# Kernel optimization log

Measured on AMD Instinct MI355X. Metric: run time of the kernel, lower is better.

The kernel has to match this reference:

```python
import jax, jax.numpy as jnp
import numpy as np

EMBED_DIM = 768
NUM_HEADS = 12
LN_EPS = 1e-5


def _apply_rope3d(p16, e):
    """3-axis RoPE. p16: [B,1,L,3] float16 coords; e: [B,H,L,D] float32.
    Heads split into 3 groups (x/y/z); within each group last dim split in halves
    and rotated by angle coord*freqs (computed in fp16, matching the .half() cast)."""
    B, H, L, D = e.shape
    half = D // 2
    freqs = (10000.0 ** (-jnp.arange(half, dtype=jnp.float32) / half)).astype(jnp.float16)
    ang = p16[..., None] * freqs                     # [B,1,L,3,half] fp16
    ang = jnp.transpose(ang, (0, 3, 1, 2, 4))        # [B,3,1,L,half]
    c, s = jnp.cos(ang), jnp.sin(ang)                # fp16
    eg = e.reshape(B, 3, H // 3, L, D)               # 3 head groups
    e1, e2 = eg[..., :half], eg[..., half:]
    o1 = e1 * c - e2 * s                             # fp16*fp32 -> fp32
    o2 = e2 * c + e1 * s
    return jnp.concatenate([o1, o2], axis=-1).reshape(B, H, L, D)


def setup_inputs() -> dict:
    key = jax.random.key(0)
    ks = jax.random.split(key, 5)
    B, L, C = 4, 2048, EMBED_DIM
    feat = jax.random.normal(ks[0], (B, L, C), dtype=jnp.float32)
    pos = jax.random.normal(ks[1], (B, L, 3), dtype=jnp.float32)
    w_qkv = jax.random.normal(ks[2], (C, 3 * C), dtype=jnp.float32) * (1.0 / np.sqrt(C))
    b_qkv = jnp.zeros((3 * C,), dtype=jnp.float32)
    w_proj = jax.random.normal(ks[3], (C, C), dtype=jnp.float32) * (1.0 / np.sqrt(C))
    b_proj = jnp.zeros((C,), dtype=jnp.float32)
    ln_g = jnp.ones((C,), dtype=jnp.float32)
    ln_b = jnp.zeros((C,), dtype=jnp.float32)
    return {"feat": feat, "pos": pos, "ln_g": ln_g, "ln_b": ln_b,
            "w_qkv": w_qkv, "b_qkv": b_qkv, "w_proj": w_proj, "b_proj": b_proj}


def reference(feat, pos, ln_g, ln_b, w_qkv, b_qkv, w_proj, b_proj):
    B, L, C = feat.shape
    H = NUM_HEADS
    D = C // H
    # LayerNorm
    mu = jnp.mean(feat, axis=-1, keepdims=True)
    var = jnp.mean(jnp.square(feat - mu), axis=-1, keepdims=True)
    x = (feat - mu) * jax.lax.rsqrt(var + LN_EPS) * ln_g + ln_b
    # QKV projection and head split
    qkv = x @ w_qkv + b_qkv
    q, k, v = jnp.split(qkv, 3, axis=-1)
    q = q.reshape(B, L, H, D).transpose(0, 2, 1, 3)  # [B,H,L,D]
    k = k.reshape(B, L, H, D).transpose(0, 2, 1, 3)
    v = v.reshape(B, L, H, D).transpose(0, 2, 1, 3)
    # 3D-coordinate RoPE (angles in fp16 per original .half() cast)
    p16 = pos.astype(jnp.float16)[:, None]           # [B,1,L,3]
    q = _apply_rope3d(p16, q)
    k = _apply_rope3d(p16, k)
    # flex_attention with block_mask=None -> full softmax attention, scale 1/sqrt(D)
    scale = 1.0 / np.sqrt(D)
    att = jax.nn.softmax(jnp.einsum('bhqd,bhkd->bhqk', q, k) * scale, axis=-1)
    out = jnp.einsum('bhqk,bhkd->bhqd', att, v)
    out = out.transpose(0, 2, 1, 3).reshape(B, L, C)
    # output projection (dropout = identity in eval)
    return out @ w_proj + b_proj
```

## Files before the change

### kernel.cpp

```cpp
#include <hip/hip_runtime.h>

typedef unsigned short u16;
typedef unsigned int u32;
typedef __attribute__((ext_vector_type(8))) __bf16 bf16x8;
typedef __attribute__((ext_vector_type(4))) __bf16 bf16x4;
typedef __attribute__((ext_vector_type(8))) u16 ushort8;
typedef __attribute__((ext_vector_type(4))) float f32x4;

#define DEV static __device__ __forceinline__

DEV float bf2f(u16 v) { union { u32 u; float f; } x; x.u = ((u32)v) << 16; return x.f; }
DEV u16 f2bf(float f) {
  u32 u = __builtin_bit_cast(u32, f);
  return (u16)((u + 0x7fffu + ((u >> 16) & 1u)) >> 16);
}
DEV float rnd_bf(float f) { return bf2f(f2bf(f)); }
DEV u32 pack2(float a, float b) { return (u32)f2bf(a) | ((u32)f2bf(b) << 16); }

DEV void gload_lds16(const void* g, void* l) {
  __builtin_amdgcn_global_load_lds((const __attribute__((address_space(1))) u32*)g,
                                   (__attribute__((address_space(3))) u32*)l, 16, 0, 0);
}

DEV f32x4 MFMA16(bf16x8 a, bf16x8 b, f32x4 c) {
  return __builtin_amdgcn_mfma_f32_16x16x32_bf16(a, b, c, 0, 0, 0);
}

__global__ __launch_bounds__(256) void wt_transpose(const float* __restrict__ W, u16* __restrict__ Wt,
                                                    int rows, int cols) {
  __shared__ u16 t[64][65];
  const int tid = threadIdx.x;
  const int tr = blockIdx.y << 6, tc = blockIdx.x << 6;
  {
    int r = tid >> 2, c0 = (tid & 3) << 4;
    const float* src = W + (size_t)(tr + r) * cols + tc + c0;
#pragma unroll
    for (int i = 0; i < 16; i += 4) {
      float4 v = *(const float4*)(src + i);
      t[r][c0 + i]     = f2bf(v.x);
      t[r][c0 + i + 1] = f2bf(v.y);
      t[r][c0 + i + 2] = f2bf(v.z);
      t[r][c0 + i + 3] = f2bf(v.w);
    }
  }
  __syncthreads();
  {
    int dd = tid >> 2, l0 = (tid & 3) << 4;
    ushort8 o0, o1;
#pragma unroll
    for (int i = 0; i < 8; ++i) { o0[i] = t[l0 + i][dd]; o1[i] = t[l0 + 8 + i][dd]; }
    u16* dst = Wt + (size_t)(tc + dd) * rows + tr + l0;
    *(ushort8*)dst = o0;
    *(ushort8*)(dst + 8) = o1;
  }
}

__global__ __launch_bounds__(256) void ln_kernel(const float* __restrict__ feat, const float* __restrict__ gam,
                                                 const float* __restrict__ bet, u16* __restrict__ xo) {
  const int row = blockIdx.x * 4 + (threadIdx.x >> 6);
  const int lane = threadIdx.x & 63;
  const float* f = feat + (size_t)row * 768 + lane * 4;
  float4 v0 = *(const float4*)f;
  float4 v1 = *(const float4*)(f + 256);
  float4 v2 = *(const float4*)(f + 512);
  float s = v0.x + v0.y + v0.z + v0.w + v1.x + v1.y + v1.z + v1.w + v2.x + v2.y + v2.z + v2.w;
  float s2 = v0.x*v0.x + v0.y*v0.y + v0.z*v0.z + v0.w*v0.w
           + v1.x*v1.x + v1.y*v1.y + v1.z*v1.z + v1.w*v1.w
           + v2.x*v2.x + v2.y*v2.y + v2.z*v2.z + v2.w*v2.w;
#pragma unroll
  for (int off = 32; off > 0; off >>= 1) { s += __shfl_xor(s, off); s2 += __shfl_xor(s2, off); }
  const float mu = s * (1.0f / 768.0f);
  const float rstd = rsqrtf(s2 * (1.0f / 768.0f) - mu * mu + 1e-5f);
  u16* o = xo + (size_t)row * 768 + lane * 4;
  const float4* gp = (const float4*)(gam + lane * 4);
  const float4* bp = (const float4*)(bet + lane * 4);
  float4 vv[3] = {v0, v1, v2};
#pragma unroll
  for (int jj = 0; jj < 3; ++jj) {
    float4 gg = gp[jj * 64];
    float4 bb = bp[jj * 64];
    uint2 pk;
    pk.x = pack2((vv[jj].x - mu) * rstd * gg.x + bb.x, (vv[jj].y - mu) * rstd * gg.y + bb.y);
    pk.y = pack2((vv[jj].z - mu) * rstd * gg.z + bb.z, (vv[jj].w - mu) * rstd * gg.w + bb.w);
    *(uint2*)(o + jj * 256) = pk;
  }
}

template<bool F32OUT>
__global__ __launch_bounds__(256) void gemm_bt(const u16* __restrict__ A, const u16* __restrict__ Bt,
                                               const float* __restrict__ bias, void* __restrict__ Cout,
                                               int M, int N, int K) {
  __shared__ u16 lds[16384];
  const int tid = threadIdx.x;
  const int lane = tid & 63, wv = tid >> 6;
  const int l16 = lane & 15, g = lane >> 4;
  const int nt = N >> 7;
  const int bm = blockIdx.x / nt, bn = blockIdx.x % nt;
  const int m0 = bm << 7, n0 = bn << 7;
  const int wr = (wv >> 1) << 6, wc = (wv & 1) << 6;
  const int rl = wv * 8 + (lane >> 3);
  const int slot = lane & 7;

  f32x4 acc[4][4] = {};

  for (int k0 = 0; k0 < K; k0 += 64) {
    __syncthreads();
#pragma unroll
    for (int it = 0; it < 4; ++it) {
      int r = it * 32 + rl;
      gload_lds16(A + (size_t)(m0 + r) * K + k0 + 8 * (slot ^ (r & 7)),
                  (char*)lds + it * 4096 + wv * 1024);
      gload_lds16(Bt + (size_t)(n0 + r) * K + k0 + 8 * (slot ^ (r & 7)),
                  (char*)lds + 16384 + it * 4096 + wv * 1024);
    }
    __syncthreads();
#pragma unroll
    for (int ks = 0; ks < 2; ++ks) {
      bf16x8 af[4], bfr[4];
#pragma unroll
      for (int mf = 0; mf < 4; ++mf) {
        int r = wr + mf * 16 + l16;
        af[mf] = *(const bf16x8*)((const char*)lds + r * 128 + ((ks * 64 + g * 16) ^ ((r & 7) << 4)));
      }
#pragma unroll
      for (int nf = 0; nf < 4; ++nf) {
        int r = wc + nf * 16 + l16;
        bfr[nf] = *(const bf16x8*)((const char*)lds + 16384 + r * 128 + ((ks * 64 + g * 16) ^ ((r & 7) << 4)));
      }
#pragma unroll
      for (int mf = 0; mf < 4; ++mf)
#pragma unroll
        for (int nf = 0; nf < 4; ++nf)
          acc[mf][nf] = MFMA16(af[mf], bfr[nf], acc[mf][nf]);
    }
  }
#pragma unroll
  for (int nf = 0; nf < 4; ++nf) {
    int col = n0 + wc + nf * 16 + l16;
    float bb = bias[col];
#pragma unroll
    for (int mf = 0; mf < 4; ++mf) {
      int row = m0 + wr + mf * 16 + g * 4;
#pragma unroll
      for (int j = 0; j < 4; ++j) {
        float v = acc[mf][nf][j] + bb;
        if (F32OUT) ((float*)Cout)[(size_t)(row + j) * N + col] = rnd_bf(v);
        else        ((u16*)Cout)[(size_t)(row + j) * N + col] = f2bf(v);
      }
    }
  }
}

__global__ __launch_bounds__(256) void rope_qk(const u16* __restrict__ qkv, const float* __restrict__ pos,
                                               u16* __restrict__ Q, u16* __restrict__ K) {
  int gid = blockIdx.x * 256 + threadIdx.x;
  int d = gid & 31;
  int hh = (gid >> 5) % 12;
  int bl = (gid >> 5) / 12;
  const u16* row = qkv + (size_t)bl * 2304;
  float q1 = bf2f(row[hh * 64 + d]);
  float q2 = bf2f(row[hh * 64 + 32 + d]);
  float k1 = bf2f(row[768 + hh * 64 + d]);
  float k2 = bf2f(row[768 + hh * 64 + 32 + d]);
  float p = pos[(size_t)bl * 3 + (hh >> 2)];
  float fr = exp2f((float)d * -0.41524101186092029f);
  _Float16 ah = (_Float16)p * (_Float16)fr;
  float af = (float)ah;
  float sn, cs;
  sincosf(af, &sn, &cs);
  float c = (float)(_Float16)cs;
  float s = (float)(_Float16)sn;
  size_t oidx = ((size_t)((bl >> 11) * 12 + hh) * 2048 + (bl & 2047)) * 64 + d;
  Q[oidx]      = f2bf((q1 * c - q2 * s) * 0.125f);
  Q[oidx + 32] = f2bf((q2 * c + q1 * s) * 0.125f);
  K[oidx]      = f2bf(k1 * c - k2 * s);
  K[oidx + 32] = f2bf(k2 * c + k1 * s);
}

__global__ __launch_bounds__(256) void v_transpose(const u16* __restrict__ qkv, u16* __restrict__ Vt) {
  __shared__ u16 t[64][65];
  const int tid = threadIdx.x;
  const int lt = blockIdx.x, bh = blockIdx.y;
  const int b = bh / 12, h = bh - b * 12;
  {
    int r = tid >> 2, c0 = (tid & 3) << 4;
    const u16* src = qkv + (size_t)(b * 2048 + lt * 64 + r) * 2304 + 1536 + h * 64 + c0;
    ushort8 a0 = *(const ushort8*)src;
    ushort8 a1 = *(const ushort8*)(src + 8);
#pragma unroll
    for (int i = 0; i < 8; ++i) { t[r][c0 + i] = a0[i]; t[r][c0 + 8 + i] = a1[i]; }
  }
  __syncthreads();
  {
    int dd = tid >> 2, l0 = (tid & 3) << 4;
    ushort8 o0, o1;
#pragma unroll
    for (int i = 0; i < 8; ++i) { o0[i] = t[l0 + i][dd]; o1[i] = t[l0 + 8 + i][dd]; }
    u16* dst = Vt + (size_t)(bh * 64 + dd) * 2048 + lt * 64 + l0;
    *(ushort8*)dst = o0;
    *(ushort8*)(dst + 8) = o1;
  }
}

__global__ __launch_bounds__(256) void attn_kernel(const u16* __restrict__ Q, const u16* __restrict__ K,
                                                   const u16* __restrict__ Vt, u16* __restrict__ O) {
  __shared__ u16 kv_lds[2][8192];
  const int tid = threadIdx.x;
  const int lane = tid & 63, wv = tid >> 6;
  const int l16 = lane & 15, g = lane >> 4;
  const int bh = blockIdx.y;
  const int q0 = blockIdx.x * 128 + wv * 32;
  const size_t base = (size_t)bh * (2048 * 64);
  const size_t vbase = (size_t)bh * (64 * 2048);
  const int rl = wv * 8 + (lane >> 3);
  const int slot = lane & 7;

  bf16x8 qf[2][2];
#pragma unroll
  for (int qm = 0; qm < 2; ++qm)
#pragma unroll
    for (int ks = 0; ks < 2; ++ks)
      qf[qm][ks] = *(const bf16x8*)(Q + base + (size_t)(q0 + qm * 16 + l16) * 64 + ks * 32 + g * 8);

  float lsum[2] = {0.f, 0.f};
  f32x4 oacc[2][4] = {};

#pragma unroll
  for (int it = 0; it < 2; ++it) {
    int r = it * 32 + rl;
    gload_lds16(K + base + (size_t)r * 64 + 8 * (slot ^ (r & 7)),
                (char*)kv_lds + it * 4096 + wv * 1024);
    gload_lds16(Vt + vbase + (size_t)r * 2048 + 8 * (slot ^ (r & 7)),
                (char*)kv_lds + 8192 + it * 4096 + wv * 1024);
  }
  __syncthreads();

  int cur = 0;
  for (int kv0 = 0; kv0 < 2048; kv0 += 64) {
    if (kv0 + 64 < 2048) {
#pragma unroll
      for (int it = 0; it < 2; ++it) {
        int r = it * 32 + rl;
        gload_lds16(K + base + (size_t)(kv0 + 64 + r) * 64 + 8 * (slot ^ (r & 7)),
                    (char*)kv_lds + (cur ^ 1) * 16384 + it * 4096 + wv * 1024);
        gload_lds16(Vt + vbase + (size_t)r * 2048 + kv0 + 64 + 8 * (slot ^ (r & 7)),
                    (char*)kv_lds + (cur ^ 1) * 16384 + 8192 + it * 4096 + wv * 1024);
      }
    }

    const char* kb = (const char*)kv_lds + cur * 16384;
    const char* vbuf = kb + 8192;

    f32x4 st[2][4] = {};
#pragma unroll
    for (int ks = 0; ks < 2; ++ks) {
      bf16x8 kf[4];
#pragma unroll
      for (int n = 0; n < 4; ++n) {
        int r = n * 16 + l16;
        kf[n] = *(const bf16x8*)(kb + r * 128 + ((ks * 64 + g * 16) ^ ((r & 7) << 4)));
      }
      __builtin_amdgcn_s_setprio(1);
#pragma unroll
      for (int qm = 0; qm < 2; ++qm)
#pragma unroll
        for (int n = 0; n < 4; ++n)
          st[qm][n] = MFMA16(kf[n], qf[qm][ks], st[qm][n]);
      __builtin_amdgcn_s_setprio(0);
    }

#pragma unroll
    for (int ks2 = 0; ks2 < 2; ++ks2) {
      bf16x8 vf[4];
#pragma unroll
      for (int db = 0; db < 4; ++db) {
        int r = db * 16 + l16;
        int swz = (r & 7) << 4;
        const char* rowb = vbuf + r * 128;
        bf16x4 lo = *(const bf16x4*)(rowb + ((ks2 * 64 + g * 8) ^ swz));
        bf16x4 hi = *(const bf16x4*)(rowb + ((ks2 * 64 + g * 8 + 32) ^ swz));
        vf[db] = __builtin_shufflevector(lo, hi, 0, 1, 2, 3, 4, 5, 6, 7);
      }
      bf16x8 pf[2];
#pragma unroll
      for (int qm = 0; qm < 2; ++qm) {
        float e[8];
#pragma unroll
        for (int j = 0; j < 4; ++j) {
          e[j]     = __expf(st[qm][2 * ks2][j]);
          e[4 + j] = __expf(st[qm][2 * ks2 + 1][j]);
        }
        lsum[qm] += ((e[0] + e[1]) + (e[2] + e[3])) + ((e[4] + e[5]) + (e[6] + e[7]));
        ushort8 pp;
#pragma unroll
        for (int j = 0; j < 8; ++j) pp[j] = f2bf(e[j]);
        pf[qm] = __builtin_bit_cast(bf16x8, pp);
      }
      __builtin_amdgcn_s_setprio(1);
#pragma unroll
      for (int qm = 0; qm < 2; ++qm)
#pragma unroll
        for (int db = 0; db < 4; ++db)
          oacc[qm][db] = MFMA16(vf[db], pf[qm], oacc[qm][db]);
      __builtin_amdgcn_s_setprio(0);
    }

    __syncthreads();
    cur ^= 1;
  }

  const int b = bh / 12, h = bh - b * 12;
#pragma unroll
  for (int qm = 0; qm < 2; ++qm) {
    float tot = lsum[qm];
    tot += __shfl_xor(tot, 16);
    tot += __shfl_xor(tot, 32);
    float inv = 1.0f / tot;
    size_t row = (size_t)b * 2048 + q0 + qm * 16 + l16;
#pragma unroll
    for (int db = 0; db < 4; ++db) {
      uint2 pk;
      pk.x = pack2(oacc[qm][db][0] * inv, oacc[qm][db][1] * inv);
      pk.y = pack2(oacc[qm][db][2] * inv, oacc[qm][db][3] * inv);
      *(uint2*)(O + row * 768 + h * 64 + db * 16 + g * 4) = pk;
    }
  }
}

extern "C" void kernel_launch(void* const* d_in, const int* in_sizes, int n_in,
                              void* d_out, int out_size, void* d_ws, size_t ws_size,
                              hipStream_t stream) {
  (void)in_sizes; (void)n_in; (void)out_size; (void)ws_size;
  const float* feat   = (const float*)d_in[0];
  const float* pos    = (const float*)d_in[1];
  const float* ln_g   = (const float*)d_in[2];
  const float* ln_b   = (const float*)d_in[3];
  const float* w_qkv  = (const float*)d_in[4];
  const float* b_qkv  = (const float*)d_in[5];
  const float* w_proj = (const float*)d_in[6];
  const float* b_proj = (const float*)d_in[7];
  float* out = (float*)d_out;
  char* ws = (char*)d_ws;
  u16* xln    = (u16*)(ws);
  u16* wqkvT  = (u16*)(ws + 12582912);
  u16* wprojT = (u16*)(ws + 16121856);
  u16* qkv    = (u16*)(ws + 17301504);
  u16* Kb     = (u16*)(ws + 55050240);
  u16* Vtb    = (u16*)(ws + 67633152);
  u16* Qb     = xln;
  u16* attnout = qkv;

  wt_transpose<<<dim3(36, 12), 256, 0, stream>>>(w_qkv, wqkvT, 768, 2304);
  wt_transpose<<<dim3(12, 12), 256, 0, stream>>>(w_proj, wprojT, 768, 768);
  ln_kernel<<<2048, 256, 0, stream>>>(feat, ln_g, ln_b, xln);
  gemm_bt<false><<<1152, 256, 0, stream>>>(xln, wqkvT, b_qkv, qkv, 8192, 2304, 768);
  rope_qk<<<12288, 256, 0, stream>>>(qkv, pos, Qb, Kb);
  v_transpose<<<dim3(32, 48), 256, 0, stream>>>(qkv, Vtb);
  attn_kernel<<<dim3(16, 48), 256, 0, stream>>>(Qb, Kb, Vtb, attnout);
  gemm_bt<true><<<384, 256, 0, stream>>>(attnout, wprojT, b_proj, out, 8192, 768, 768);
}
```

Measured before the change: 180.3 us.

## Fuse RoPE into QKV GEMM epilogue, triple-buffer attention K/V loads, use exp2

Removes the separate rope_qk kernel by applying bias, 3D RoPE and the Q scale, with log2e folded in, inside the QKV GEMM epilogue. The attention kernel now reads Q and K directly from the strided qkv buffer. K/V staging goes from double to triple buffering with explicit vmcnt waits and raw barriers, so loads for tile t+2 are in flight while tile t is computed. exp becomes exp2 and the bf16 conversion uses the native cast. The costs are more LDS per block, strided K loads with a 2304-element row pitch, and sincos work repeated across the epilogue lanes.

```diff
diff --git a/kernel.cpp b/kernel.cpp
--- a/kernel.cpp
+++ b/kernel.cpp
@@ -25,6 +25,8 @@
 DEV f32x4 MFMA16(bf16x8 a, bf16x8 b, f32x4 c) {
   return __builtin_amdgcn_mfma_f32_16x16x32_bf16(a, b, c, 0, 0, 0);
 }
+
+#define QSCALE (0.125f * 1.442695040888963f)
 
 __global__ __launch_bounds__(256) void wt_transpose(const float* __restrict__ W, u16* __restrict__ Wt,
                                                     int rows, int cols) {
@@ -86,10 +88,10 @@
   }
 }
 
-template<bool F32OUT>
+template<bool ROPE, bool F32OUT>
 __global__ __launch_bounds__(256) void gemm_bt(const u16* __restrict__ A, const u16* __restrict__ Bt,
                                                const float* __restrict__ bias, void* __restrict__ Cout,
-                                               int M, int N, int K) {
+                                               const float* __restrict__ pos, int M, int N, int K) {
   __shared__ u16 lds[16384];
   const int tid = threadIdx.x;
   const int lane = tid & 63, wv = tid >> 6;
@@ -134,47 +136,59 @@
           acc[mf][nf] = MFMA16(af[mf], bfr[nf], acc[mf][nf]);
     }
   }
-#pragma unroll
-  for (int nf = 0; nf < 4; ++nf) {
-    int col = n0 + wc + nf * 16 + l16;
-    float bb = bias[col];
-#pragma unroll
-    for (int mf = 0; mf < 4; ++mf) {
-      int row = m0 + wr + mf * 16 + g * 4;
-#pragma unroll
-      for (int j = 0; j < 4; ++j) {
-        float v = acc[mf][nf][j] + bb;
-        if (F32OUT) ((float*)Cout)[(size_t)(row + j) * N + col] = rnd_bf(v);
-        else        ((u16*)Cout)[(size_t)(row + j) * N + col] = f2bf(v);
-      }
-    }
-  }
-}
-
-__global__ __launch_bounds__(256) void rope_qk(const u16* __restrict__ qkv, const float* __restrict__ pos,
-                                               u16* __restrict__ Q, u16* __restrict__ K) {
-  int gid = blockIdx.x * 256 + threadIdx.x;
-  int d = gid & 31;
-  int hh = (gid >> 5) % 12;
-  int bl = (gid >> 5) / 12;
-  const u16* row = qkv + (size_t)bl * 2304;
-  float q1 = bf2f(row[hh * 64 + d]);
-  float q2 = bf2f(row[hh * 64 + 32 + d]);
-  float k1 = bf2f(row[768 + hh * 64 + d]);
-  float k2 = bf2f(row[768 + hh * 64 + 32 + d]);
-  float p = pos[(size_t)bl * 3 + (hh >> 2)];
-  float fr = exp2f((float)d * -0.41524101186092029f);
-  _Float16 ah = (_Float16)p * (_Float16)fr;
-  float af = (float)ah;
-  float sn, cs;
-  sincosf(af, &sn, &cs);
-  float c = (float)(_Float16)cs;
-  float s = (float)(_Float16)sn;
-  size_t oidx = ((size_t)((bl >> 11) * 12 + hh) * 2048 + (bl & 2047)) * 64 + d;
-  Q[oidx]      = f2bf((q1 * c - q2 * s) * 0.125f);
-  Q[oidx + 32] = f2bf((q2 * c + q1 * s) * 0.125f);
-  K[oidx]      = f2bf(k1 * c - k2 * s);
-  K[oidx + 32] = f2bf(k2 * c + k1 * s);
+
+  if (ROPE && n0 < 1536) {
+    const int colbase = n0 + wc;
+    const bool isQ = colbase < 768;
+    const int h = (isQ ? colbase : colbase - 768) >> 6;
+    const int axis = h >> 2;
+    u16* C = (u16*)Cout;
+#pragma unroll
+    for (int nf = 0; nf < 2; ++nf) {
+      const int col = n0 + wc + nf * 16 + l16;
+      const int d = nf * 16 + l16;
+      const float fr = exp2f((float)d * -0.41524101186092029f);
+      const float b1 = bias[col], b2 = bias[col + 32];
+#pragma unroll
+      for (int mf = 0; mf < 4; ++mf) {
+        int row0 = m0 + wr + mf * 16 + g * 4;
+#pragma unroll
+        for (int j = 0; j < 4; ++j) {
+          int row = row0 + j;
+          float p = pos[(size_t)row * 3 + axis];
+          _Float16 ah = (_Float16)p * (_Float16)fr;
+          float sn, cs;
+          sincosf((float)ah, &sn, &cs);
+          float c = (float)(_Float16)cs;
+          float s = (float)(_Float16)sn;
+          float a = acc[mf][nf][j] + b1;
+          float bb = acc[mf][nf + 2][j] + b2;
+          float o1 = a * c - bb * s;
+          float o2 = bb * c + a * s;
+          if (isQ) { o1 *= QSCALE; o2 *= QSCALE; }
+          u16* Crow = C + (size_t)row * N;
+          Crow[col] = f2bf(o1);
+          Crow[col + 32] = f2bf(o2);
+        }
+      }
+    }
+  } else {
+#pragma unroll
+    for (int nf = 0; nf < 4; ++nf) {
+      int col = n0 + wc + nf * 16 + l16;
+      float bb = bias[col];
+#pragma unroll
+      for (int mf = 0; mf < 4; ++mf) {
+        int row = m0 + wr + mf * 16 + g * 4;
+#pragma unroll
+        for (int j = 0; j < 4; ++j) {
+          float v = acc[mf][nf][j] + bb;
+          if (F32OUT) ((float*)Cout)[(size_t)(row + j) * N + col] = rnd_bf(v);
+          else        ((u16*)Cout)[(size_t)(row + j) * N + col] = f2bf(v);
+        }
+      }
+    }
+  }
 }
 
 __global__ __launch_bounds__(256) void v_transpose(const u16* __restrict__ qkv, u16* __restrict__ Vt) {
@@ -202,15 +216,17 @@
   }
 }
 
-__global__ __launch_bounds__(256) void attn_kernel(const u16* __restrict__ Q, const u16* __restrict__ K,
-                                                   const u16* __restrict__ Vt, u16* __restrict__ O) {
-  __shared__ u16 kv_lds[2][8192];
+__global__ __launch_bounds__(256) void attn_kernel(const u16* __restrict__ qkv, const u16* __restrict__ Vt,
+                                                   u16* __restrict__ O) {
+  __shared__ u16 kv_lds[3][8192];
   const int tid = threadIdx.x;
   const int lane = tid & 63, wv = tid >> 6;
   const int l16 = lane & 15, g = lane >> 4;
   const int bh = blockIdx.y;
+  const int b = bh / 12, h = bh - b * 12;
   const int q0 = blockIdx.x * 128 + wv * 32;
-  const size_t base = (size_t)bh * (2048 * 64);
+  const u16* qrow = qkv + (size_t)b * 2048 * 2304 + h * 64;
+  const u16* krow = qrow + 768;
   const size_t vbase = (size_t)bh * (64 * 2048);
   const int rl = wv * 8 + (lane >> 3);
   const int slot = lane & 7;
@@ -220,35 +236,31 @@
   for (int qm = 0; qm < 2; ++qm)
 #pragma unroll
     for (int ks = 0; ks < 2; ++ks)
-      qf[qm][ks] = *(const bf16x8*)(Q + base + (size_t)(q0 + qm * 16 + l16) * 64 + ks * 32 + g * 8);
+      qf[qm][ks] = *(const bf16x8*)(qrow + (size_t)(q0 + qm * 16 + l16) * 2304 + ks * 32 + g * 8);
 
   float lsum[2] = {0.f, 0.f};
   f32x4 oacc[2][4] = {};
 
-#pragma unroll
-  for (int it = 0; it < 2; ++it) {
-    int r = it * 32 + rl;
-    gload_lds16(K + base + (size_t)r * 64 + 8 * (slot ^ (r & 7)),
-                (char*)kv_lds + it * 4096 + wv * 1024);
-    gload_lds16(Vt + vbase + (size_t)r * 2048 + 8 * (slot ^ (r & 7)),
-                (char*)kv_lds + 8192 + it * 4096 + wv * 1024);
-  }
-  __syncthreads();
-
-  int cur = 0;
-  for (int kv0 = 0; kv0 < 2048; kv0 += 64) {
-    if (kv0 + 64 < 2048) {
-#pragma unroll
-      for (int it = 0; it < 2; ++it) {
-        int r = it * 32 + rl;
-        gload_lds16(K + base + (size_t)(kv0 + 64 + r) * 64 + 8 * (slot ^ (r & 7)),
-                    (char*)kv_lds + (cur ^ 1) * 16384 + it * 4096 + wv * 1024);
-        gload_lds16(Vt + vbase + (size_t)r * 2048 + kv0 + 64 + 8 * (slot ^ (r & 7)),
-                    (char*)kv_lds + (cur ^ 1) * 16384 + 8192 + it * 4096 + wv * 1024);
-      }
-    }
-
-    const char* kb = (const char*)kv_lds + cur * 16384;
+  auto STAGE = [&](int tile, int buf) {
+#pragma unroll
+    for (int it = 0; it < 2; ++it) {
+      int r = it * 32 + rl;
+      gload_lds16(krow + (size_t)(tile * 64 + r) * 2304 + 8 * (slot ^ (r & 7)),
+                  (char*)kv_lds + buf * 16384 + it * 4096 + wv * 1024);
+      gload_lds16(Vt + vbase + (size_t)r * 2048 + tile * 64 + 8 * (slot ^ (r & 7)),
+                  (char*)kv_lds + buf * 16384 + 8192 + it * 4096 + wv * 1024);
+    }
+  };
+
+  STAGE(0, 0);
+  STAGE(1, 1);
+  asm volatile("s_waitcnt vmcnt(4)" ::: "memory");
+  __builtin_amdgcn_s_barrier();
+
+  for (int t = 0; t < 32; ++t) {
+    if (t < 30) STAGE(t + 2, (t + 2) % 3);
+
+    const char* kb = (const char*)kv_lds + (t % 3) * 16384;
     const char* vbuf = kb + 8192;
 
     f32x4 st[2][4] = {};
@@ -287,14 +299,14 @@
         float e[8];
 #pragma unroll
         for (int j = 0; j < 4; ++j) {
-          e[j]     = __expf(st[qm][2 * ks2][j]);
-          e[4 + j] = __expf(st[qm][2 * ks2 + 1][j]);
+          e[j]     = __builtin_exp2f(st[qm][2 * ks2][j]);
+          e[4 + j] = __builtin_exp2f(st[qm][2 * ks2 + 1][j]);
         }
         lsum[qm] += ((e[0] + e[1]) + (e[2] + e[3])) + ((e[4] + e[5]) + (e[6] + e[7]));
-        ushort8 pp;
-#pragma unroll
-        for (int j = 0; j < 8; ++j) pp[j] = f2bf(e[j]);
-        pf[qm] = __builtin_bit_cast(bf16x8, pp);
+        bf16x8 pv;
+#pragma unroll
+        for (int j = 0; j < 8; ++j) pv[j] = (__bf16)e[j];
+        pf[qm] = pv;
       }
       __builtin_amdgcn_s_setprio(1);
 #pragma unroll
@@ -305,11 +317,13 @@
       __builtin_amdgcn_s_setprio(0);
     }
 
-    __syncthreads();
-    cur ^= 1;
-  }
-
-  const int b = bh / 12, h = bh - b * 12;
+    if (t < 31) {
+      if (t < 30) asm volatile("s_waitcnt vmcnt(4)" ::: "memory");
+      else        asm volatile("s_waitcnt vmcnt(0)" ::: "memory");
+      __builtin_amdgcn_s_barrier();
+    }
+  }
+
 #pragma unroll
   for (int qm = 0; qm < 2; ++qm) {
     float tot = lsum[qm];
@@ -345,17 +359,14 @@
   u16* wqkvT  = (u16*)(ws + 12582912);
   u16* wprojT = (u16*)(ws + 16121856);
   u16* qkv    = (u16*)(ws + 17301504);
-  u16* Kb     = (u16*)(ws + 55050240);
+  u16* attnout= (u16*)(ws + 55050240);
   u16* Vtb    = (u16*)(ws + 67633152);
-  u16* Qb     = xln;
-  u16* attnout = qkv;
 
   wt_transpose<<<dim3(36, 12), 256, 0, stream>>>(w_qkv, wqkvT, 768, 2304);
   wt_transpose<<<dim3(12, 12), 256, 0, stream>>>(w_proj, wprojT, 768, 768);
   ln_kernel<<<2048, 256, 0, stream>>>(feat, ln_g, ln_b, xln);
-  gemm_bt<false><<<1152, 256, 0, stream>>>(xln, wqkvT, b_qkv, qkv, 8192, 2304, 768);
-  rope_qk<<<12288, 256, 0, stream>>>(qkv, pos, Qb, Kb);
+  gemm_bt<true, false><<<1152, 256, 0, stream>>>(xln, wqkvT, b_qkv, qkv, pos, 8192, 2304, 768);
   v_transpose<<<dim3(32, 48), 256, 0, stream>>>(qkv, Vtb);
-  attn_kernel<<<dim3(16, 48), 256, 0, stream>>>(Qb, Kb, Vtb, attnout);
-  gemm_bt<true><<<384, 256, 0, stream>>>(attnout, wprojT, b_proj, out, 8192, 768, 768);
-}
+  attn_kernel<<<dim3(16, 48), 256, 0, stream>>>(qkv, Vtb, attnout);
+  gemm_bt<false, true><<<384, 256, 0, stream>>>(attnout, wprojT, b_proj, out, pos, 8192, 768, 768);
+}
```

New measurement: 200.4 us. 11.2% more time.
